# Performance work log

Measured on AMD Instinct MI355X. Metric: run time of the kernel, lower is better.

Reference implementation:

```python
import jax, jax.numpy as jnp
import numpy as np

K_TOPK = 16
TEMP = 1.0
NUM_HEADS = 16


def setup_inputs() -> dict:
    key = jax.random.key(0)
    ks = jax.random.split(key, 10)
    B, N, C = 2, 2048, 512
    return {
        "query": jax.random.normal(ks[0], (B, N, C), jnp.float32),
        "key": jax.random.normal(ks[1], (B, N, C), jnp.float32),
        "value": jax.random.normal(ks[2], (B, N, C), jnp.float32),
        "pos_embedding": jax.random.normal(ks[3], (B, N, C), jnp.float32),
        "noise": jax.random.uniform(ks[4], (B, N, N), jnp.float32),
        "w_qkv": jax.random.normal(ks[5], (3 * C, C), jnp.float32) * (1.0 / np.sqrt(C)),
        "b_qkv": jax.random.normal(ks[6], (3 * C,), jnp.float32) * 0.02,
        "w_proj": jax.random.normal(ks[7], (C, C), jnp.float32) * (1.0 / np.sqrt(C)),
        "b_proj": jax.random.normal(ks[8], (C,), jnp.float32) * 0.02,
        "head_scores": jnp.ones((NUM_HEADS,), jnp.float32),
    }


def reference(query, key, value, pos_embedding, noise, w_qkv, b_qkv, w_proj, b_proj, head_scores):
    # query/key/pos_embedding are unused in the executed torch forward path.
    B, N, C = value.shape
    H = NUM_HEADS
    dh = C // H
    qkv = value @ w_qkv.T + b_qkv                     # [B,N,3C]
    qkv = qkv.reshape(B, N, 3, H, dh).transpose(2, 0, 3, 1, 4)  # [3,B,H,N,dh]
    q, k, v = qkv[0], qkv[1], qkv[2]

    scale = 1.0 / np.sqrt(dh)
    scores = jnp.einsum("bhnd,bhmd->bhnm", q, k) * scale       # [B,H,N,N]

    # Gumbel top-K gate (same scores math as torch: q@k^T/sqrt(dh) mean over heads)
    logits = scores.mean(axis=1)                                # [B,N,N]
    gumbel = -jnp.log(-jnp.log(noise + 1e-9) + 1e-9)
    probs = jax.nn.softmax((logits + gumbel) / TEMP, axis=-1)
    topk_vals = jax.lax.top_k(probs, K_TOPK)[0]                 # sorted desc
    thresh = topk_vals[..., -1:]                                # min of top-K
    sparse_mask = (probs >= thresh).astype(scores.dtype)[:, None]  # [B,1,N,N]

    attn = jax.nn.softmax(scores, axis=-1) * sparse_mask
    out = jnp.einsum("bhnm,bhmd->bhnd", attn, v)                # [B,H,N,dh]
    out = out.transpose(0, 2, 1, 3).reshape(B, N, C)
    out = out * head_scores.mean()
    return out @ w_proj.T + b_proj
```

## Files before the change

kernel.cpp:

```cpp
#include <hip/hip_runtime.h>
#include <hip/hip_bf16.h>

#define NB 2
#define NN 2048
#define NC 512
#define NH 16
#define NDH 32
#define NROWS (NB * NN)
#define KTOP 16

#define SCALE 0.17677669529663687f
#define SCALE16 0.011048543456039804f

typedef __attribute__((ext_vector_type(8))) short bf16x8;
typedef __attribute__((ext_vector_type(4))) float f32x4;

#define GLD16(g, l)                                                      \
  __builtin_amdgcn_global_load_lds(                                      \
      (const __attribute__((address_space(1))) void*)(g),                \
      (__attribute__((address_space(3))) void*)(l), 16, 0, 0)

__global__ __launch_bounds__(256) void split_kernel(
    const float* __restrict__ val, const float* __restrict__ wq,
    const float* __restrict__ wp, __hip_bfloat16* __restrict__ valsp,
    __hip_bfloat16* __restrict__ wqsp, __hip_bfloat16* __restrict__ wpsp) {
  const int row = blockIdx.x * 2 + (threadIdx.x >> 7);
  const int kc = (threadIdx.x & 127) * 4;
  const float* src;
  __hip_bfloat16* dst;
  int rr;
  if (row < 4096) {
    src = val; dst = valsp; rr = row;
  } else if (row < 5632) {
    src = wq; dst = wqsp; rr = row - 4096;
  } else {
    src = wp; dst = wpsp; rr = row - 5632;
  }
  float4 x = *(const float4*)&src[(size_t)rr * 512 + kc];
  float xs[4] = {x.x, x.y, x.z, x.w};
#pragma unroll
  for (int j = 0; j < 4; j++) {
    __hip_bfloat16 hi = __float2bfloat16(xs[j]);
    __hip_bfloat16 lo = __float2bfloat16(xs[j] - __bfloat162float(hi));
    dst[(size_t)rr * 1024 + kc + j] = hi;
    dst[(size_t)rr * 1024 + 512 + kc + j] = lo;
  }
}

template <int EPI>
__global__ __launch_bounds__(256, 2) void gemm_bf16s(
    const __hip_bfloat16* __restrict__ Aspg, int lda,
    const __hip_bfloat16* __restrict__ Bspg, int ldb,
    const float* __restrict__ bias, const float* __restrict__ noise,
    const float* __restrict__ hsp, float* __restrict__ Cc, int ldc,
    float* __restrict__ qkvf, __hip_bfloat16* __restrict__ Qsp,
    __hip_bfloat16* __restrict__ Ksp, __hip_bfloat16* __restrict__ Khm) {
  __shared__ short As[128 * 64];
  __shared__ short Bs[128 * 64];
  const int t = threadIdx.x;
  const int lane = t & 63;
  const int wv = t >> 6;
  const int wr = wv >> 1, wc = wv & 1;
  const int bm = blockIdx.y * 128;
  const int bn = blockIdx.x * 128;
  const short* Asp = (const short*)Aspg;
  const short* Bsp = (const short*)Bspg;
  if constexpr (EPI == 2) Bsp += (size_t)(bm >> 11) * 2048 * (size_t)ldb;

  const int r = lane & 15, g = lane >> 4;
  const int srow = t >> 3;
  const int scol = (t & 7) * 8;

  f32x4 acc[4][4];
#pragma unroll
  for (int m = 0; m < 4; m++)
#pragma unroll
    for (int n = 0; n < 4; n++) acc[m][n] = {0.f, 0.f, 0.f, 0.f};

  for (int s = 0; s < 24; s++) {
    const int pass = s >> 3;
    const int k0 = (s & 7) * 64;
    const int aoff = (pass == 2) ? 512 : 0;
    const int boff = (pass == 1) ? 512 : 0;
    __syncthreads();
#pragma unroll
    for (int i = 0; i < 4; i++) {
      GLD16(Asp + (size_t)(bm + i * 32 + srow) * lda + aoff + k0 + scol,
            &As[i * 2048 + t * 8]);
      GLD16(Bsp + (size_t)(bn + i * 32 + srow) * ldb + boff + k0 + scol,
            &Bs[i * 2048 + t * 8]);
    }
    __syncthreads();
    bf16x8 af[4][2], bfr[4][2];
#pragma unroll
    for (int m = 0; m < 4; m++)
#pragma unroll
      for (int ks = 0; ks < 2; ks++)
        af[m][ks] =
            *(const bf16x8*)&As[(wr * 64 + m * 16 + r) * 64 + ks * 32 + g * 8];
#pragma unroll
    for (int n = 0; n < 4; n++)
#pragma unroll
      for (int ks = 0; ks < 2; ks++)
        bfr[n][ks] =
            *(const bf16x8*)&Bs[(wc * 64 + n * 16 + r) * 64 + ks * 32 + g * 8];
#pragma unroll
    for (int m = 0; m < 4; m++)
#pragma unroll
      for (int n = 0; n < 4; n++) {
        acc[m][n] = __builtin_amdgcn_mfma_f32_16x16x32_bf16(
            af[m][0], bfr[n][0], acc[m][n], 0, 0, 0);
        acc[m][n] = __builtin_amdgcn_mfma_f32_16x16x32_bf16(
            af[m][1], bfr[n][1], acc[m][n], 0, 0, 0);
      }
  }

  float hs = 1.0f;
  if constexpr (EPI == 3) {
    float ssum = 0.f;
#pragma unroll
    for (int i = 0; i < NH; i++) ssum += hsp[i];
    hs = ssum * (1.0f / NH);
  }

#pragma unroll
  for (int m = 0; m < 4; m++)
#pragma unroll
    for (int n = 0; n < 4; n++)
#pragma unroll
      for (int j = 0; j < 4; j++) {
        const int row = bm + wr * 64 + m * 16 + g * 4 + j;
        const int col = bn + wc * 64 + n * 16 + r;
        float x = acc[m][n][j];
        if constexpr (EPI == 1) {
          x += bias[col];
          qkvf[(size_t)row * 1536 + col] = x;
          if (col < 1024) {
            __hip_bfloat16 hi = __float2bfloat16(x);
            __hip_bfloat16 lo = __float2bfloat16(x - __bfloat162float(hi));
            __hip_bfloat16* dst = (col < 512) ? Qsp : Ksp;
            const int c = col & 511;
            dst[(size_t)row * 1024 + c] = hi;
            dst[(size_t)row * 1024 + c + 512] = lo;
            if (col >= 512) {
              const int kc = col - 512;
              Khm[((size_t)(kc >> 5) * NROWS + row) * NDH + (kc & 31)] = hi;
            }
          }
        } else if constexpr (EPI == 2) {
          const int bb = row >> 11;
          const int nr = row & (NN - 1);
          float u = noise[((size_t)bb << 22) + ((size_t)nr << 11) + col];
          float gum = -logf(-logf(u + 1e-9f) + 1e-9f);
          Cc[(size_t)row * ldc + col] = x * SCALE16 + gum;
        } else {
          Cc[(size_t)row * ldc + col] = x * hs + bias[col];
        }
      }
}

__global__ __launch_bounds__(256) void topk_kernel(
    const float* __restrict__ z, unsigned long long* __restrict__ mask) {
  const int lane = threadIdx.x & 63;
  const int row = blockIdx.x * 4 + (threadIdx.x >> 6);
  const float* zr = z + (size_t)row * NN;

  float v[32];
#pragma unroll
  for (int r = 0; r < 32; r++) v[r] = zr[r * 64 + lane];

  float lmax = v[0];
#pragma unroll
  for (int r = 1; r < 32; r++) lmax = fmaxf(lmax, v[r]);

  float thresh = 0.f;
  for (int it = 0; it < KTOP; it++) {
    float m = lmax;
#pragma unroll
    for (int s = 1; s < 64; s <<= 1) m = fmaxf(m, __shfl_xor(m, s));
    thresh = m;
    const unsigned long long ball = __ballot(lmax == m);
    if (lane == (int)__builtin_ctzll(ball)) {
      bool done = false;
#pragma unroll
      for (int r = 0; r < 32; r++) {
        const bool hit = !done && (v[r] == m);
        if (hit) v[r] = -INFINITY;
        done = done || hit;
      }
      lmax = v[0];
#pragma unroll
      for (int r = 1; r < 32; r++) lmax = fmaxf(lmax, v[r]);
    }
  }

  unsigned long long mword = 0ull;
#pragma unroll
  for (int r = 0; r < 32; r++) {
    const unsigned long long bal = __ballot(zr[r * 64 + lane] >= thresh);
    if (lane == r) mword = bal;
  }
  if (lane < 32) mask[(size_t)row * 32 + lane] = mword;
}

__global__ __launch_bounds__(256) void denom_kernel(
    const __hip_bfloat16* __restrict__ Qsp, const __hip_bfloat16* __restrict__ Khm,
    float* __restrict__ Zpart) {
  const int lane = threadIdx.x & 63;
  const int wave = threadIdx.x >> 6;
  const int rowbase = blockIdx.x * 64 + wave * 16;
  const int h = blockIdx.y;
  const int chunk = blockIdx.z;
  const int b = rowbase >> 11;
  const int rl = lane & 15;
  const int g = lane >> 4;

  const short* qb = (const short*)Qsp;
  bf16x8 afrag =
      *(const bf16x8*)&qb[(size_t)(rowbase + rl) * 1024 + h * NDH + g * 8];
  const short* kb = (const short*)Khm +
                    ((size_t)h * NROWS + (b << 11) + chunk * 1024) * NDH;
  float sum[4] = {0.f, 0.f, 0.f, 0.f};
  for (int m0 = 0; m0 < 1024; m0 += 32) {
    bf16x8 b0 = *(const bf16x8*)&kb[(m0 + rl) * NDH + g * 8];
    bf16x8 b1 = *(const bf16x8*)&kb[(m0 + 16 + rl) * NDH + g * 8];
    f32x4 zero = {0.f, 0.f, 0.f, 0.f};
    f32x4 d0 =
        __builtin_amdgcn_mfma_f32_16x16x32_bf16(afrag, b0, zero, 0, 0, 0);
    f32x4 d1 =
        __builtin_amdgcn_mfma_f32_16x16x32_bf16(afrag, b1, zero, 0, 0, 0);
#pragma unroll
    for (int j = 0; j < 4; j++)
      sum[j] += __expf(d0[j] * SCALE) + __expf(d1[j] * SCALE);
  }
#pragma unroll
  for (int j = 0; j < 4; j++)
#pragma unroll
    for (int s = 1; s < 16; s <<= 1) sum[j] += __shfl_xor(sum[j], s);
  if (rl == 0) {
#pragma unroll
    for (int j = 0; j < 4; j++) {
      const int row = rowbase + g * 4 + j;
      Zpart[((size_t)chunk << 16) + (size_t)row * NH + h] = sum[j];
    }
  }
}

__global__ __launch_bounds__(256) void gather_kernel(
    const float* __restrict__ qkv, const float* __restrict__ Zpart,
    const unsigned long long* __restrict__ mask,
    __hip_bfloat16* __restrict__ aosp) {
  const int t = threadIdx.x;
  const int lane = t & 63;
  const int wave = t >> 6;
  const int l32 = lane & 31;
  const int rhalf = lane >> 5;
  const int row = blockIdx.x * 8 + wave * 2 + rhalf;
  const int h = blockIdx.y;
  const int b = row >> 11;
  const int rloc = wave * 2 + rhalf;

  __shared__ int idxbuf[8][64];
  __shared__ int cnts[8];

  const unsigned long long* mrow = mask + (size_t)row * 32;
  unsigned long long bits = mrow[l32];
  int c = __popcll(bits);
  int p = c;
#pragma unroll
  for (int d = 1; d < 32; d <<= 1) {
    int o = __shfl_up(p, d, 32);
    if (l32 >= d) p += o;
  }
  int total = __shfl(p, 31, 32);
  p -= c;
  while (bits) {
    int tz = __builtin_ctzll(bits);
    bits &= bits - 1;
    if (p < 64) idxbuf[rloc][p] = (l32 << 6) + tz;
    p++;
  }
  if (l32 == 0) cnts[rloc] = total > 64 ? 64 : total;
  __syncthreads();
  const int cnt = cnts[rloc];

  const int chb = h * NDH + (l32 & 1) * 16;
  const float* qrow = qkv + (size_t)row * 1536 + chb;
  float q0[16];
#pragma unroll
  for (int i = 0; i < 4; i++)
    *(float4*)&q0[i * 4] = *(const float4*)&qrow[i * 4];
  const float* Kf = qkv + (size_t)(b << 11) * 1536 + 512 + chb;
  const float* Vf = qkv + (size_t)(b << 11) * 1536 + 1024 + chb;
  float acc[16] = {};
  for (int base = 0; base < cnt; base += 16) {
    const int hit = base + (l32 >> 1);
    const bool valid = hit < cnt;
    const int m = valid ? idxbuf[rloc][hit] : 0;
    const float* kr = Kf + (size_t)m * 1536;
    float part = 0.f;
#pragma unroll
    for (int i = 0; i < 4; i++) {
      float4 kv4 = *(const float4*)&kr[i * 4];
      part = fmaf(q0[i * 4 + 0], kv4.x, part);
      part = fmaf(q0[i * 4 + 1], kv4.y, part);
      part = fmaf(q0[i * 4 + 2], kv4.z, part);
      part = fmaf(q0[i * 4 + 3], kv4.w, part);
    }
    part += __shfl_xor(part, 1);
    const float pexp = valid ? __expf(part * SCALE) : 0.f;
    const float* vr = Vf + (size_t)m * 1536;
#pragma unroll
    for (int i = 0; i < 4; i++) {
      float4 vv4 = *(const float4*)&vr[i * 4];
      acc[i * 4 + 0] = fmaf(pexp, vv4.x, acc[i * 4 + 0]);
      acc[i * 4 + 1] = fmaf(pexp, vv4.y, acc[i * 4 + 1]);
      acc[i * 4 + 2] = fmaf(pexp, vv4.z, acc[i * 4 + 2]);
      acc[i * 4 + 3] = fmaf(pexp, vv4.w, acc[i * 4 + 3]);
    }
  }
#pragma unroll
  for (int s = 2; s < 32; s <<= 1)
#pragma unroll
    for (int ch = 0; ch < 16; ch++) acc[ch] += __shfl_xor(acc[ch], s);

  if (l32 < 2) {
    const float Z = Zpart[(size_t)row * NH + h] +
                    Zpart[(1 << 16) + (size_t)row * NH + h];
    const float Zinv = 1.0f / Z;
#pragma unroll
    for (int ch = 0; ch < 16; ch++) {
      const float v = acc[ch] * Zinv;
      __hip_bfloat16 hi = __float2bfloat16(v);
      __hip_bfloat16 lo = __float2bfloat16(v - __bfloat162float(hi));
      aosp[(size_t)row * 1024 + chb + ch] = hi;
      aosp[(size_t)row * 1024 + 512 + chb + ch] = lo;
    }
  }
}

extern "C" void kernel_launch(void* const* d_in, const int* in_sizes, int n_in,
                              void* d_out, int out_size, void* d_ws,
                              size_t ws_size, hipStream_t stream) {
  const float* value = (const float*)d_in[2];
  const float* noise = (const float*)d_in[4];
  const float* w_qkv = (const float*)d_in[5];
  const float* b_qkv = (const float*)d_in[6];
  const float* w_proj = (const float*)d_in[7];
  const float* b_proj = (const float*)d_in[8];
  const float* head_scores = (const float*)d_in[9];
  float* out = (float*)d_out;

  char* ws = (char*)d_ws;
  size_t o = 0;
  float* qkv = (float*)(ws + o);                 o += (size_t)NROWS * 1536 * 4;
  __hip_bfloat16* Qsp = (__hip_bfloat16*)(ws + o); o += (size_t)NROWS * 1024 * 2;
  __hip_bfloat16* Ksp = (__hip_bfloat16*)(ws + o); o += (size_t)NROWS * 1024 * 2;
  __hip_bfloat16* wpsp = (__hip_bfloat16*)(ws + o); o += (size_t)512 * 1024 * 2;
  unsigned long long* mask = (unsigned long long*)(ws + o); o += (size_t)NROWS * 32 * 8;
  __hip_bfloat16* aosp = (__hip_bfloat16*)(ws + o); o += (size_t)NROWS * 1024 * 2;
  float* z = (float*)(ws + o);                   o += (size_t)NROWS * NN * 4;
  float* Zpart = (float*)(ws + o);               o += (size_t)2 * NROWS * NH * 4;
  __hip_bfloat16* valsp = (__hip_bfloat16*)z;
  __hip_bfloat16* wqsp = (__hip_bfloat16*)((char*)z + 8388608);
  __hip_bfloat16* Khm = aosp;

  split_kernel<<<3072, 256, 0, stream>>>(value, w_qkv, w_proj, valsp, wqsp,
                                         wpsp);
  gemm_bf16s<1><<<dim3(12, 32), 256, 0, stream>>>(
      valsp, 1024, wqsp, 1024, b_qkv, nullptr, nullptr, nullptr, 0, qkv, Qsp,
      Ksp, Khm);
  gemm_bf16s<2><<<dim3(16, 32), 256, 0, stream>>>(
      Qsp, 1024, Ksp, 1024, nullptr, noise, nullptr, z, NN, nullptr, nullptr,
      nullptr, nullptr);
  topk_kernel<<<NROWS / 4, 256, 0, stream>>>(z, mask);
  denom_kernel<<<dim3(64, 16, 2), 256, 0, stream>>>(Qsp, Khm, Zpart);
  gather_kernel<<<dim3(NROWS / 8, NH), 256, 0, stream>>>(qkv, Zpart, mask,
                                                         aosp);
  gemm_bf16s<3><<<dim3(4, 32), 256, 0, stream>>>(
      aosp, 1024, wpsp, 1024, b_proj, nullptr, head_scores, out, NC, nullptr,
      nullptr, nullptr, nullptr);
}
```

Baseline: 324.0 us.

## Load hi/lo split tiles together and XOR-swizzle LDS layout in split-bf16 GEMM

```diff
diff --git a/kernel.cpp b/kernel.cpp
--- a/kernel.cpp
+++ b/kernel.cpp
@@ -55,8 +55,10 @@
     const float* __restrict__ hsp, float* __restrict__ Cc, int ldc,
     float* __restrict__ qkvf, __hip_bfloat16* __restrict__ Qsp,
     __hip_bfloat16* __restrict__ Ksp, __hip_bfloat16* __restrict__ Khm) {
-  __shared__ short As[128 * 64];
-  __shared__ short Bs[128 * 64];
+  __shared__ short Ah[128 * 64];
+  __shared__ short Al[128 * 64];
+  __shared__ short Bh[128 * 64];
+  __shared__ short Bl[128 * 64];
   const int t = threadIdx.x;
   const int lane = t & 63;
   const int wv = t >> 6;
@@ -69,7 +71,7 @@
 
   const int r = lane & 15, g = lane >> 4;
   const int srow = t >> 3;
-  const int scol = (t & 7) * 8;
+  const int scol = (((t & 7) ^ ((t >> 3) & 7)) * 8);
 
   f32x4 acc[4][4];
 #pragma unroll
@@ -77,33 +79,65 @@
 #pragma unroll
     for (int n = 0; n < 4; n++) acc[m][n] = {0.f, 0.f, 0.f, 0.f};
 
-  for (int s = 0; s < 24; s++) {
-    const int pass = s >> 3;
-    const int k0 = (s & 7) * 64;
-    const int aoff = (pass == 2) ? 512 : 0;
-    const int boff = (pass == 1) ? 512 : 0;
+  const int rx = r & 7;
+
+  for (int s = 0; s < 8; s++) {
+    const int k0 = s * 64;
     __syncthreads();
 #pragma unroll
     for (int i = 0; i < 4; i++) {
-      GLD16(Asp + (size_t)(bm + i * 32 + srow) * lda + aoff + k0 + scol,
-            &As[i * 2048 + t * 8]);
-      GLD16(Bsp + (size_t)(bn + i * 32 + srow) * ldb + boff + k0 + scol,
-            &Bs[i * 2048 + t * 8]);
+      const size_t ar = (size_t)(bm + i * 32 + srow) * lda + k0 + scol;
+      const size_t br = (size_t)(bn + i * 32 + srow) * ldb + k0 + scol;
+      GLD16(Asp + ar, &Ah[i * 2048 + t * 8]);
+      GLD16(Asp + ar + 512, &Al[i * 2048 + t * 8]);
+      GLD16(Bsp + br, &Bh[i * 2048 + t * 8]);
+      GLD16(Bsp + br + 512, &Bl[i * 2048 + t * 8]);
     }
     __syncthreads();
+
     bf16x8 af[4][2], bfr[4][2];
 #pragma unroll
     for (int m = 0; m < 4; m++)
 #pragma unroll
       for (int ks = 0; ks < 2; ks++)
-        af[m][ks] =
-            *(const bf16x8*)&As[(wr * 64 + m * 16 + r) * 64 + ks * 32 + g * 8];
+        af[m][ks] = *(const bf16x8*)&Ah[(wr * 64 + m * 16 + r) * 64 +
+                                        ((ks * 4 + g) ^ rx) * 8];
 #pragma unroll
     for (int n = 0; n < 4; n++)
 #pragma unroll
       for (int ks = 0; ks < 2; ks++)
-        bfr[n][ks] =
-            *(const bf16x8*)&Bs[(wc * 64 + n * 16 + r) * 64 + ks * 32 + g * 8];
+        bfr[n][ks] = *(const bf16x8*)&Bl[(wc * 64 + n * 16 + r) * 64 +
+                                         ((ks * 4 + g) ^ rx) * 8];
+#pragma unroll
+    for (int m = 0; m < 4; m++)
+#pragma unroll
+      for (int n = 0; n < 4; n++) {
+        acc[m][n] = __builtin_amdgcn_mfma_f32_16x16x32_bf16(
+            af[m][0], bfr[n][0], acc[m][n], 0, 0, 0);
+        acc[m][n] = __builtin_amdgcn_mfma_f32_16x16x32_bf16(
+            af[m][1], bfr[n][1], acc[m][n], 0, 0, 0);
+      }
+#pragma unroll
+    for (int n = 0; n < 4; n++)
+#pragma unroll
+      for (int ks = 0; ks < 2; ks++)
+        bfr[n][ks] = *(const bf16x8*)&Bh[(wc * 64 + n * 16 + r) * 64 +
+                                         ((ks * 4 + g) ^ rx) * 8];
+#pragma unroll
+    for (int m = 0; m < 4; m++)
+#pragma unroll
+      for (int n = 0; n < 4; n++) {
+        acc[m][n] = __builtin_amdgcn_mfma_f32_16x16x32_bf16(
+            af[m][0], bfr[n][0], acc[m][n], 0, 0, 0);
+        acc[m][n] = __builtin_amdgcn_mfma_f32_16x16x32_bf16(
+            af[m][1], bfr[n][1], acc[m][n], 0, 0, 0);
+      }
+#pragma unroll
+    for (int m = 0; m < 4; m++)
+#pragma unroll
+      for (int ks = 0; ks < 2; ks++)
+        af[m][ks] = *(const bf16x8*)&Al[(wr * 64 + m * 16 + r) * 64 +
+                                        ((ks * 4 + g) ^ rx) * 8];
 #pragma unroll
     for (int m = 0; m < 4; m++)
 #pragma unroll
```

Result: faster. 284.0 us (-12.4%).
